# Kernel optimization log

Measured on AMD Instinct MI355X. Metric: run time of the kernel, lower is better.

## Reference

```python
import jax, jax.numpy as jnp
import numpy as np

D_STATE = 64
D_CONV = 5
HEADDIM = 64
EXPAND = 2


def setup_inputs() -> dict:
    key = jax.random.key(0)
    ks = jax.random.split(key, 12)
    b, ch, h, w = 4, 128, 64, 64
    d_inner = EXPAND * ch
    nheads = d_inner // HEADDIM
    conv_ch = d_inner + 2 * D_STATE
    d_in_proj = 2 * d_inner + 2 * D_STATE + nheads
    s = lambda k, shape, scale: jax.random.normal(k, shape, jnp.float32) * scale
    return {
        "noisy": s(ks[0], (b, ch, h, w), 1.0),
        "aux": s(ks[1], (b, ch, h, w), 1.0),
        "ln_gamma": jnp.ones((ch,), jnp.float32),
        "ln_beta": jnp.zeros((ch,), jnp.float32),
        "in_proj_w": s(ks[2], (d_in_proj, ch), ch ** -0.5),
        "conv_w": s(ks[3], (conv_ch, D_CONV), D_CONV ** -0.5),
        "conv_b": s(ks[4], (conv_ch,), 0.02),
        "A_log": jnp.log(jnp.linspace(1.0, 16.0, nheads)).astype(jnp.float32),
        "dt_bias": s(ks[5], (nheads,), 0.1),
        "D": jnp.ones((nheads,), jnp.float32),
        "rms_w": jnp.ones((d_inner,), jnp.float32),
        "out_proj_w": s(ks[6], (ch, d_inner), d_inner ** -0.5),
        "ff_w1": s(ks[7], (ch, ch, 3, 3), (ch * 9) ** -0.5),
        "ff_b1": jnp.zeros((ch,), jnp.float32),
        "ff_w2": s(ks[8], (ch, ch, 3, 3), (ch * 9) ** -0.5),
        "ff_b2": jnp.zeros((ch,), jnp.float32),
    }


def _mamba2(u, in_proj_w, conv_w, conv_b, A_log, dt_bias, D_skip, rms_w, out_proj_w):
    # u: (b, L, d_model). Mamba2 with ngroups=1, headdim=64.
    b, L, d = u.shape
    d_inner = EXPAND * d
    nheads = d_inner // HEADDIM
    zxbcdt = u @ in_proj_w.T  # (b, L, 2*d_inner + 2*d_state + nheads)
    z = zxbcdt[..., :d_inner]
    xBC = zxbcdt[..., d_inner:2 * d_inner + 2 * D_STATE]
    dt = jax.nn.softplus(zxbcdt[..., -nheads:] + dt_bias)  # (b, L, h)
    # causal depthwise conv1d along L + SiLU
    xBC_c = jnp.transpose(xBC, (0, 2, 1))  # (b, C, L)
    xBC_c = jax.lax.conv_general_dilated(
        xBC_c, conv_w[:, None, :], (1,), [(D_CONV - 1, 0)],
        feature_group_count=xBC_c.shape[1])
    xBC = jax.nn.silu(jnp.transpose(xBC_c + conv_b[None, :, None], (0, 2, 1)))
    x = xBC[..., :d_inner]
    B = xBC[..., d_inner:d_inner + D_STATE]  # (b, L, n)
    C = xBC[..., d_inner + D_STATE:]         # (b, L, n)
    A = -jnp.exp(A_log)                      # (h,)
    xh = x.reshape(b, L, nheads, HEADDIM)    # (b, L, h, p)
    dA = jnp.exp(dt * A)                     # (b, L, h)

    def step(hstate, inputs):
        dA_t, dt_t, x_t, B_t, C_t = inputs
        hstate = hstate * dA_t[:, :, None, None] + jnp.einsum('bh,bhp,bn->bhpn', dt_t, x_t, B_t)
        y_t = jnp.einsum('bhpn,bn->bhp', hstate, C_t)
        return hstate, y_t

    init = jnp.zeros((b, nheads, HEADDIM, D_STATE), u.dtype)
    xs = (jnp.moveaxis(dA, 1, 0), jnp.moveaxis(dt, 1, 0), jnp.moveaxis(xh, 1, 0),
          jnp.moveaxis(B, 1, 0), jnp.moveaxis(C, 1, 0))
    _, ys = jax.lax.scan(step, init, xs)
    y = jnp.moveaxis(ys, 0, 1) + xh * D_skip[None, None, :, None]  # (b, L, h, p)
    y = y.reshape(b, L, d_inner)
    # gated RMSNorm: rmsnorm(y * silu(z)) * weight
    y = y * jax.nn.silu(z)
    y = y * jax.lax.rsqrt(jnp.mean(y * y, axis=-1, keepdims=True) + 1e-5) * rms_w
    return y @ out_proj_w.T


def _conv3x3_reflect(x, w, b):
    x = jnp.pad(x, ((0, 0), (0, 0), (1, 1), (1, 1)), mode='reflect')
    return jax.lax.conv_general_dilated(x, w, (1, 1), 'VALID') + b[None, :, None, None]


def reference(noisy, aux, ln_gamma, ln_beta, in_proj_w, conv_w, conv_b, A_log,
              dt_bias, D, rms_w, out_proj_w, ff_w1, ff_b1, ff_w2, ff_b2):
    b, c, h, w = noisy.shape
    flat = jnp.transpose(noisy, (0, 2, 3, 1)).reshape(b, h * w, c)
    mu = jnp.mean(flat, axis=-1, keepdims=True)
    var = jnp.var(flat, axis=-1, keepdims=True)
    normed = (flat - mu) * jax.lax.rsqrt(var + 1e-5) * ln_gamma + ln_beta
    m = _mamba2(normed, in_proj_w, conv_w, conv_b, A_log, dt_bias, D, rms_w, out_proj_w)
    m = jnp.transpose(m.reshape(b, h, w, c), (0, 3, 1, 2))
    y = noisy + m
    ff = jax.nn.relu(_conv3x3_reflect(y, ff_w1, ff_b1))
    ff = jax.nn.relu(_conv3x3_reflect(ff, ff_w2, ff_b2))
    y = y + ff
    return (y, aux)
```

## Files before the change

### kernel.cpp

```cpp
#include <hip/hip_runtime.h>
#include <cstddef>

#define B_      4
#define C_      128
#define L_      4096
#define DIN     256
#define NH      4
#define HD      64
#define DS      64
#define CONVCH  384
#define DPROJ   644
#define CHUNK   64
#define NCHUNK  64

typedef short bf16x8 __attribute__((ext_vector_type(8)));
typedef float floatx16 __attribute__((ext_vector_type(16)));

__device__ __forceinline__ float siluf(float v) { return v / (1.f + __expf(-v)); }

__device__ __forceinline__ ushort f2bf(float v) {
  unsigned u = __float_as_uint(v);
  unsigned r = (u + 0x7fff + ((u >> 16) & 1)) >> 16;
  return (ushort)r;
}
__device__ __forceinline__ float bf2f(ushort h) {
  return __uint_as_float((unsigned)h << 16);
}

__device__ __forceinline__ void split8(float4 v0, float4 v1, bf16x8& hi, bf16x8& lo) {
  float f[8] = {v0.x, v0.y, v0.z, v0.w, v1.x, v1.y, v1.z, v1.w};
#pragma unroll
  for (int j = 0; j < 8; ++j) {
    ushort h = f2bf(f[j]);
    hi[j] = (short)h;
    lo[j] = (short)f2bf(f[j] - bf2f(h));
  }
}

__global__ __launch_bounds__(256) void wprep_all(
    const float* __restrict__ ipw, ushort* __restrict__ Bh, ushort* __restrict__ Bl,
    const float* __restrict__ opw, ushort* __restrict__ Oh, ushort* __restrict__ Ol,
    const float* __restrict__ fw1, ushort* __restrict__ Wt1,
    const float* __restrict__ fw2, ushort* __restrict__ Wt2) {
  int bi = blockIdx.x;
  int t = threadIdx.x;
  if (bi < 176) {
    int e = bi * 256 + t;
    int d = e >> 6;
    int c0 = (e & 63) * 2;
    int kk = c0 >> 4;
    int l = (d & 31) + 32 * ((c0 & 15) >> 3);
    int j = c0 & 7;
    size_t off = (((size_t)(d >> 5)) * 8 + kk) * 512 + l * 8 + j;
    float v0 = d < 644 ? ipw[(size_t)d * 128 + c0] : 0.f;
    float v1 = d < 644 ? ipw[(size_t)d * 128 + c0 + 1] : 0.f;
    ushort h0 = f2bf(v0), h1 = f2bf(v1);
    *(unsigned*)(Bh + off) = (unsigned)h0 | ((unsigned)h1 << 16);
    *(unsigned*)(Bl + off) = (unsigned)f2bf(v0 - bf2f(h0)) |
                             ((unsigned)f2bf(v1 - bf2f(h1)) << 16);
  } else if (bi < 304) {
    int e = (bi - 176) * 256 + t;
    int d = e >> 8;
    int c = e & 255;
    size_t f = ((size_t)(d >> 5) * 16 + (c >> 4)) * 512 +
               ((d & 31) + 32 * ((c & 15) >> 3)) * 8 + (c & 7);
    float v = opw[(size_t)d * 256 + c];
    ushort h = f2bf(v);
    Oh[f] = h;
    Ol[f] = f2bf(v - bf2f(h));
  } else {
    const float* fw = bi < 432 ? fw1 : fw2;
    ushort* Wt = bi < 432 ? Wt1 : Wt2;
    int co = (bi - 304) & 127;
    int cb = co >> 5;
    for (int e = t; e < 1152; e += 256) {
      int tap = e >> 7;
      int ci = e & 127;
      int kk = ci >> 4, k16 = ci & 15;
      int l = (co & 31) + 32 * (k16 >> 3);
      int off = ((tap * 8 + kk) * 4 + cb) * 512 + l * 8 + (k16 & 7);
      Wt[off] = f2bf(fw[(size_t)co * 1152 + ci * 9 + tap]);
    }
  }
}

__global__ __launch_bounds__(1024) void ln_gemm1(
    const float* __restrict__ noisy, const float* __restrict__ gamma,
    const float* __restrict__ beta,
    const ushort* __restrict__ Bh, const ushort* __restrict__ Bl,
    float* __restrict__ ZX) {
  int row = blockIdx.x, b = blockIdx.y;
  int t = threadIdx.x;
  __shared__ float tile[64 * 129];
  __shared__ float ps[16][64], pq[16][64];
  __shared__ float smu[64], srs[64];
  __shared__ __align__(16) ushort AhL[8192];
  __shared__ __align__(16) ushort AlL[8192];
  int px = t & 63, cg = t >> 6;
  float s = 0.f, s2 = 0.f;
  const float* src = noisy + ((size_t)b * C_) * L_ + row * 64;
  for (int i = 0; i < 8; ++i) {
    int c = cg * 8 + i;
    float v = src[(size_t)c * L_ + px];
    tile[px * 129 + c] = v;
    s += v; s2 += v * v;
  }
  ps[cg][px] = s; pq[cg][px] = s2;
  __syncthreads();
  if (t < 64) {
    float a = 0.f, qq = 0.f;
#pragma unroll
    for (int g = 0; g < 16; ++g) { a += ps[g][t]; qq += pq[g][t]; }
    float mu = a * (1.f / 128.f);
    float var = qq * (1.f / 128.f) - mu * mu;
    smu[t] = mu;
    srs[t] = rsqrtf(var + 1e-5f);
  }
  __syncthreads();
  for (int idx = t; idx < 4096; idx += 1024) {
    int p2 = idx >> 6;
    int c0 = (idx & 63) * 2;
    float v0 = (tile[p2 * 129 + c0] - smu[p2]) * srs[p2] * gamma[c0] + beta[c0];
    float v1 = (tile[p2 * 129 + c0 + 1] - smu[p2]) * srs[p2] * gamma[c0 + 1] + beta[c0 + 1];
    int kk = c0 >> 4;
    int l = (p2 & 31) + 32 * ((c0 & 15) >> 3);
    int j = c0 & 7;
    int off = ((p2 >> 5) * 8 + kk) * 512 + l * 8 + j;
    ushort h0 = f2bf(v0), h1 = f2bf(v1);
    *(unsigned*)(AhL + off) = (unsigned)h0 | ((unsigned)h1 << 16);
    *(unsigned*)(AlL + off) = (unsigned)f2bf(v0 - bf2f(h0)) |
                              ((unsigned)f2bf(v1 - bf2f(h1)) << 16);
  }
  __syncthreads();
  int wv = t >> 6, lane = t & 63;
  int db = wv & 1, pb = (wv >> 1) & 1, bq = wv >> 2;
  int rowadd = 4 * (lane >> 5);
  for (int bn = bq; bn < 11; bn += 4) {
    floatx16 acc;
#pragma unroll
    for (int i = 0; i < 16; ++i) acc[i] = 0.f;
    size_t bbase = ((size_t)(bn * 2 + db) * 8) * 64 + lane;
    const bf16x8* pBh = (const bf16x8*)Bh + bbase;
    const bf16x8* pBl = (const bf16x8*)Bl + bbase;
#pragma unroll
    for (int kk = 0; kk < 8; ++kk) {
      bf16x8 ah = *(const bf16x8*)(AhL + (pb * 8 + kk) * 512 + lane * 8);
      bf16x8 al = *(const bf16x8*)(AlL + (pb * 8 + kk) * 512 + lane * 8);
      bf16x8 bh = pBh[kk * 64];
      bf16x8 bl = pBl[kk * 64];
      acc = __builtin_amdgcn_mfma_f32_32x32x16_bf16(ah, bh, acc, 0, 0, 0);
      acc = __builtin_amdgcn_mfma_f32_32x32x16_bf16(al, bh, acc, 0, 0, 0);
      acc = __builtin_amdgcn_mfma_f32_32x32x16_bf16(ah, bl, acc, 0, 0, 0);
    }
    int d = bn * 64 + db * 32 + (lane & 31);
    if (d < 644) {
#pragma unroll
      for (int r = 0; r < 16; ++r) {
        int rowm = (r & 3) + 8 * (r >> 2) + rowadd;
        int pix = row * 64 + pb * 32 + rowm;
        ZX[((size_t)(b * L_ + pix)) * DPROJ + d] = acc[r];
      }
    }
  }
}

__global__ __launch_bounds__(384) void conv1d_silu(
    const float* __restrict__ ZX, const float* __restrict__ cw,
    const float* __restrict__ cb, float* __restrict__ XBC) {
  int ch = threadIdx.x;
  int l0 = blockIdx.x * 16, b = blockIdx.y;
  const float* base = ZX + ((size_t)b * L_) * DPROJ + DIN + ch;
  float w0 = cw[ch * 5], w1 = cw[ch * 5 + 1], w2 = cw[ch * 5 + 2],
        w3 = cw[ch * 5 + 3], w4 = cw[ch * 5 + 4];
  float bias = cb[ch];
  float win[20];
#pragma unroll
  for (int i = 0; i < 20; ++i) {
    int ll = l0 - 4 + i;
    win[i] = ll >= 0 ? base[(size_t)ll * DPROJ] : 0.f;
  }
  float* dst = XBC + ((size_t)(b * L_ + l0)) * CONVCH + ch;
#pragma unroll
  for (int j = 0; j < 16; ++j) {
    float acc = bias + w0 * win[j] + w1 * win[j + 1] + w2 * win[j + 2] +
                w3 * win[j + 3] + w4 * win[j + 4];
    dst[(size_t)j * CONVCH] = siluf(acc);
  }
}

#define UPDA(k, B4, C4) \
  st[4*k+0] = st[4*k+0]*da + cf*B4.x; y0 += st[4*k+0]*C4.x; \
  st[4*k+1] = st[4*k+1]*da + cf*B4.y; y1 += st[4*k+1]*C4.y; \
  st[4*k+2] = st[4*k+2]*da + cf*B4.z; y2 += st[4*k+2]*C4.z; \
  st[4*k+3] = st[4*k+3]*da + cf*B4.w; y3 += st[4*k+3]*C4.w;

__global__ __launch_bounds__(256, 4) void scan_passA(
    const float* __restrict__ XBC, const float* __restrict__ ZX,
    const float* __restrict__ dt_bias, const float* __restrict__ A_log,
    float* __restrict__ YL, float* __restrict__ SC, float* __restrict__ PC,
    float* __restrict__ CUM) {
  int chunk = blockIdx.x, h = blockIdx.y, b = blockIdx.z;
  int t = threadIdx.x;
  int p = t >> 2, q = t & 3;
  int bh = b * NH + h;
  __shared__ float sdt[CHUNK], sda[CHUNK];
  __shared__ float sB[32][64];
  __shared__ float sCc[32][64];
  __shared__ float sx[32][64];
  if (t < CHUNK) {
    int l = chunk * CHUNK + t;
    float v = ZX[((size_t)(b * L_ + l)) * DPROJ + 640 + h] + dt_bias[h];
    float dt = v > 20.f ? v : log1pf(expf(v));
    sdt[t] = dt;
    sda[t] = expf(dt * -expf(A_log[h]));
  }
  size_t rowbase = ((size_t)b * L_ + (size_t)chunk * CHUNK) * CONVCH;
  float* __restrict__ yl = YL + ((size_t)b * L_ + (size_t)chunk * CHUNK) * DIN + h * HD + p;
  float* __restrict__ cumout = CUM + (size_t)bh * L_ + chunk * CHUNK;
  float st[16];
#pragma unroll
  for (int j = 0; j < 16; ++j) st[j] = 0.f;
  float cum = 1.f;
  for (int half = 0; half < 2; ++half) {
    __syncthreads();
#pragma unroll
    for (int i = 0; i < 2; ++i) {
      int e = t + i * 256;
      int row = e >> 4, c4 = (e & 15) * 4;
      const float* gsrc = XBC + rowbase + (size_t)(half * 32 + row) * CONVCH;
      *(float4*)&sB[row][c4]  = *(const float4*)(gsrc + DIN + c4);
      *(float4*)&sCc[row][c4] = *(const float4*)(gsrc + DIN + DS + c4);
      *(float4*)&sx[row][c4]  = *(const float4*)(gsrc + h * HD + c4);
    }
    __syncthreads();
#pragma unroll 4
    for (int tl = 0; tl < 32; ++tl) {
      int tg = half * 32 + tl;
      float da = sda[tg], dtv = sdt[tg];
      float x = sx[tl][p];
      float cf = dtv * x;
      const float4* br = (const float4*)&sB[tl][q * 16];
      const float4* cr = (const float4*)&sCc[tl][q * 16];
      float4 B0 = br[0], B1 = br[1], B2 = br[2], B3 = br[3];
      float4 C0 = cr[0], C1 = cr[1], C2 = cr[2], C3 = cr[3];
      float y0 = 0.f, y1 = 0.f, y2 = 0.f, y3 = 0.f;
      UPDA(0, B0, C0) UPDA(1, B1, C1) UPDA(2, B2, C2) UPDA(3, B3, C3)
      float y = (y0 + y1) + (y2 + y3);
      y += __shfl_xor(y, 1);
      y += __shfl_xor(y, 2);
      cum *= da;
      if (q == 0) yl[(size_t)tg * DIN] = y;
      if (t == 0) cumout[tg] = cum;
    }
  }
  float* scp = SC + ((size_t)bh * NCHUNK + chunk) * 4096 + p * 64 + q * 16;
  *(float4*)(scp + 0)  = make_float4(st[0], st[1], st[2], st[3]);
  *(float4*)(scp + 4)  = make_float4(st[4], st[5], st[6], st[7]);
  *(float4*)(scp + 8)  = make_float4(st[8], st[9], st[10], st[11]);
  *(float4*)(scp + 12) = make_float4(st[12], st[13], st[14], st[15]);
  if (t == 0) PC[bh * NCHUNK + chunk] = cum;
}

__global__ __launch_bounds__(256) void scan_passB(
    float* __restrict__ SC, const float* __restrict__ PC) {
  int bh = blockIdx.x >> 4;
  int eg = blockIdx.x & 15;
  int e = eg * 256 + threadIdx.x;
  float h = 0.f;
#pragma unroll 8
  for (int c = 0; c < NCHUNK; ++c) {
    size_t idx = ((size_t)bh * NCHUNK + c) * 4096 + e;
    float s = SC[idx];
    float pcv = PC[bh * NCHUNK + c];
    SC[idx] = h;
    h = h * pcv + s;
  }
}

__global__ __launch_bounds__(1024) void passC_gate(
    const float* __restrict__ XBC, const float* __restrict__ SC,
    const float* __restrict__ CUM, const float* __restrict__ Dp,
    const float* __restrict__ YL, const float* __restrict__ ZX,
    const float* __restrict__ rmsw,
    const ushort* __restrict__ Oh, const ushort* __restrict__ Ol,
    const float* __restrict__ noisy, float* __restrict__ YRES) {
  __shared__ float yt[16384];
  __shared__ __align__(16) ushort fr[32768];
  int chunk = blockIdx.x, b = blockIdx.y;
  int t = threadIdx.x;
  int wv = t >> 6, lane = t & 63;
  size_t pix0g = (size_t)b * L_ + (size_t)chunk * CHUNK;
  float* sCcf  = (float*)fr;
  float* scumf = sCcf + 4096;

  float4 zr[4];
  {
    int lp = t & 31, slot2 = t >> 5;
#pragma unroll
    for (int it = 0; it < 2; ++it) {
      const float* z = ZX + (pix0g + it * 32 + slot2) * DPROJ;
      zr[it * 2]     = *(const float4*)(z + lp * 4);
      zr[it * 2 + 1] = *(const float4*)(z + 128 + lp * 4);
    }
  }
  for (int i = t; i < 4096; i += 1024) {
    *(float4*)&yt[i * 4] = *(const float4*)&YL[pix0g * DIN + (size_t)i * 4];
  }
  {
    int px = t >> 4, slot = t & 15;
    float4 cv = *(const float4*)(XBC + (pix0g + px) * CONVCH + DIN + DS + slot * 4);
    ((float4*)sCcf)[px * 16 + (slot ^ (px & 7))] = cv;
    if (t < 256) {
      int hh = t >> 6, px2 = t & 63;
      scumf[t] = CUM[((size_t)(b * NH + hh)) * L_ + chunk * CHUNK + px2];
    }
  }
  __syncthreads();

  {
    int px = t >> 4, c4 = (t & 15) * 4;
    const float* xs = XBC + (pix0g + px) * CONVCH;
#pragma unroll
    for (int hh = 0; hh < 4; ++hh) {
      float4 xv = *(const float4*)(xs + hh * HD + c4);
      float dv = Dp[hh];
      float* dst = &yt[px * 256 + hh * 64 + c4];
      dst[0] += xv.x * dv; dst[1] += xv.y * dv;
      dst[2] += xv.z * dv; dst[3] += xv.w * dv;
    }
  }
  __syncthreads();

  {
    int h1 = wv >> 2, ptile = (wv >> 1) & 1, pxtile = wv & 1;
    int arow = pxtile * 32 + (lane & 31);
    const float* Sb = SC + (((size_t)(b * NH + h1)) * NCHUNK + chunk) * 4096 +
                      (size_t)(ptile * 32 + (lane & 31)) * 64 + (lane >> 5) * 8;
    const float4* av = (const float4*)sCcf + arow * 16;
    int s0 = (lane >> 5) * 2;
    floatx16 acc;
#pragma unroll
    for (int i = 0; i < 16; ++i) acc[i] = 0.f;
#pragma unroll
    for (int kk = 0; kk < 4; ++kk) {
      float4 b0 = *(const float4*)(Sb + kk * 16);
      float4 b1 = *(const float4*)(Sb + kk * 16 + 4);
      int sa = kk * 4 + s0;
      float4 a0 = av[sa ^ (arow & 7)];
      float4 a1 = av[(sa + 1) ^ (arow & 7)];
      bf16x8 ah, al, bh, bl;
      split8(a0, a1, ah, al);
      split8(b0, b1, bh, bl);
      acc = __builtin_amdgcn_mfma_f32_32x32x16_bf16(ah, bh, acc, 0, 0, 0);
      acc = __builtin_amdgcn_mfma_f32_32x32x16_bf16(al, bh, acc, 0, 0, 0);
      acc = __builtin_amdgcn_mfma_f32_32x32x16_bf16(ah, bl, acc, 0, 0, 0);
    }
    int col = h1 * 64 + ptile * 32 + (lane & 31);
    int radd = 4 * (lane >> 5);
#pragma unroll
    for (int r = 0; r < 16; ++r) {
      int pxl = (r & 3) + 8 * (r >> 2) + radd;
      int px = pxtile * 32 + pxl;
      yt[px * 256 + col] += acc[r] * scumf[h1 * 64 + px];
    }
  }
  __syncthreads();

  ushort* AhL = fr;
  ushort* AlL = fr + 16384;
  {
    int lp = t & 31;
    int slot = t >> 5;
    float4 w0 = *(const float4*)(rmsw + lp * 4);
    float4 w1 = *(const float4*)(rmsw + 128 + lp * 4);
#pragma unroll
    for (int it = 0; it < 2; ++it) {
      int pl = it * 32 + slot;
      const float* y = &yt[pl * 256];
      float4 y0 = *(const float4*)(y + lp * 4);
      float4 y1 = *(const float4*)(y + 128 + lp * 4);
      float4 z0 = zr[it * 2];
      float4 z1 = zr[it * 2 + 1];
      float g[8];
      g[0] = y0.x * siluf(z0.x); g[1] = y0.y * siluf(z0.y);
      g[2] = y0.z * siluf(z0.z); g[3] = y0.w * siluf(z0.w);
      g[4] = y1.x * siluf(z1.x); g[5] = y1.y * siluf(z1.y);
      g[6] = y1.z * siluf(z1.z); g[7] = y1.w * siluf(z1.w);
      float ss = 0.f;
#pragma unroll
      for (int j = 0; j < 8; ++j) ss += g[j] * g[j];
      ss += __shfl_xor(ss, 16);
      ss += __shfl_xor(ss, 8);
      ss += __shfl_xor(ss, 4);
      ss += __shfl_xor(ss, 2);
      ss += __shfl_xor(ss, 1);
      float rs = rsqrtf(ss * (1.f / 256.f) + 1e-5f);
      float o[8];
      o[0] = g[0] * rs * w0.x; o[1] = g[1] * rs * w0.y;
      o[2] = g[2] * rs * w0.z; o[3] = g[3] * rs * w0.w;
      o[4] = g[4] * rs * w1.x; o[5] = g[5] * rs * w1.y;
      o[6] = g[6] * rs * w1.z; o[7] = g[7] * rs * w1.w;
#pragma unroll
      for (int grp = 0; grp < 2; ++grp) {
        int d = grp * 128 + lp * 4;
        int off = ((pl >> 5) * 16 + (d >> 4)) * 512 +
                  ((pl & 31) + 32 * ((d & 15) >> 3)) * 8 + (d & 7);
        ushort h0 = f2bf(o[grp*4+0]), h1 = f2bf(o[grp*4+1]);
        ushort h2 = f2bf(o[grp*4+2]), h3 = f2bf(o[grp*4+3]);
        uint2 hv, lv;
        hv.x = (unsigned)h0 | ((unsigned)h1 << 16);
        hv.y = (unsigned)h2 | ((unsigned)h3 << 16);
        lv.x = (unsigned)f2bf(o[grp*4+0] - bf2f(h0)) | ((unsigned)f2bf(o[grp*4+1] - bf2f(h1)) << 16);
        lv.y = (unsigned)f2bf(o[grp*4+2] - bf2f(h2)) | ((unsigned)f2bf(o[grp*4+3] - bf2f(h3)) << 16);
        *(uint2*)(AhL + off) = hv;
        *(uint2*)(AlL + off) = lv;
      }
    }
  }
  __syncthreads();

  floatx16 acc;
#pragma unroll
  for (int i = 0; i < 16; ++i) acc[i] = 0.f;
  int pb = wv >> 2, bn = (wv >> 1) & 1, db = wv & 1;
  int rowadd = 4 * (lane >> 5);
  if (wv < 8) {
    const bf16x8* pBh = (const bf16x8*)Oh;
    const bf16x8* pBl = (const bf16x8*)Ol;
    size_t bbase = ((size_t)(bn * 2 + db) * 16) * 64 + lane;
#pragma unroll
    for (int kk = 0; kk < 16; ++kk) {
      bf16x8 ah = *(const bf16x8*)(AhL + (pb * 16 + kk) * 512 + lane * 8);
      bf16x8 al = *(const bf16x8*)(AlL + (pb * 16 + kk) * 512 + lane * 8);
      bf16x8 bh = pBh[bbase + (size_t)kk * 64];
      bf16x8 bl = pBl[bbase + (size_t)kk * 64];
      acc = __builtin_amdgcn_mfma_f32_32x32x16_bf16(ah, bh, acc, 0, 0, 0);
      acc = __builtin_amdgcn_mfma_f32_32x32x16_bf16(al, bh, acc, 0, 0, 0);
      acc = __builtin_amdgcn_mfma_f32_32x32x16_bf16(ah, bl, acc, 0, 0, 0);
    }
  } else {
    int t2 = t - 512;
#pragma unroll
    for (int k = 0; k < 16; ++k) {
      int idx = t2 + k * 512;
      int c = idx >> 6, px = idx & 63;
      yt[idx] = noisy[((size_t)(b * C_ + c)) * L_ + chunk * CHUNK + px];
    }
  }
  __syncthreads();

  float* tile = (float*)fr;
  if (wv < 8) {
#pragma unroll
    for (int r = 0; r < 16; ++r) {
      int rowm = (r & 3) + 8 * (r >> 2) + rowadd;
      int rowp = pb * 32 + rowm;
      int col = bn * 64 + db * 32 + (lane & 31);
      tile[rowp * 129 + col] = acc[r];
    }
  }
  __syncthreads();
  for (int idx = t; idx < 8192; idx += 1024) {
    int c = idx >> 6, px = idx & 63;
    size_t o = ((size_t)(b * C_ + c)) * L_ + chunk * CHUNK + px;
    YRES[o] = yt[idx] + tile[px * 129 + c];
  }
}

template <int MODE>
__global__ __launch_bounds__(512) void conv3x3_direct(
    const void* __restrict__ inv, const ushort* __restrict__ Wt,
    const float* __restrict__ bias, const float* __restrict__ res,
    void* __restrict__ outv) {
  __shared__ __align__(16) ushort lds[3 * 64 * 128];
  int y = blockIdx.x, b = blockIdx.y;
  int t = threadIdx.x;
  int lane = t & 63;
  int wv = t >> 6;
  int ry[3];
  ry[0] = y == 0 ? 1 : y - 1;
  ry[1] = y;
  ry[2] = y == 63 ? 62 : y + 1;
  {
    int x = lane;
    for (int u = wv; u < 48; u += 8) {
      int r = u / 16;
      int cib = u % 16;
      int ci0 = cib * 8;
      ushort vals[8];
#pragma unroll
      for (int j = 0; j < 8; ++j) {
        size_t src = ((size_t)(b * C_ + ci0 + j)) * L_ + ry[r] * 64 + x;
        if (MODE == 0) vals[j] = f2bf(((const float*)inv)[src]);
        else           vals[j] = ((const ushort*)inv)[src];
      }
      int idx = (r * 64 + x) * 128 + (cib ^ (x & 15)) * 8;
      *(int4*)&lds[idx] = *(int4*)vals;
    }
  }
  __syncthreads();
  int cb = wv >> 1, nb = wv & 1;
  int n = lane & 31, hi = lane >> 5;
  floatx16 acc0, acc1;
#pragma unroll
  for (int i = 0; i < 16; ++i) { acc0[i] = 0.f; acc1[i] = 0.f; }
  const bf16x8* pW = (const bf16x8*)Wt;
  for (int tap = 0; tap < 9; ++tap) {
    int ky = tap / 3, kx = tap % 3;
    int xg = nb * 32 + n + kx - 1;
    int xx = xg < 0 ? 1 : (xg > 63 ? 62 : xg);
    int base = (ky * 64 + xx) * 128;
    int xs = xx & 15;
#pragma unroll
    for (int kk = 0; kk < 8; ++kk) {
      bf16x8 av = pW[(size_t)((tap * 8 + kk) * 4 + cb) * 64 + lane];
      bf16x8 bv = *(const bf16x8*)&lds[base + ((kk * 2 + hi) ^ xs) * 8];
      if (kk & 1) acc1 = __builtin_amdgcn_mfma_f32_32x32x16_bf16(av, bv, acc1, 0, 0, 0);
      else        acc0 = __builtin_amdgcn_mfma_f32_32x32x16_bf16(av, bv, acc0, 0, 0, 0);
    }
  }
  int x0 = nb * 32 + (lane & 31);
  int rowadd = 4 * (lane >> 5);
#pragma unroll
  for (int r = 0; r < 16; ++r) {
    int rowm = (r & 3) + 8 * (r >> 2) + rowadd;
    int co = cb * 32 + rowm;
    size_t o = ((size_t)(b * C_ + co)) * L_ + y * 64 + x0;
    float v = fmaxf(acc0[r] + acc1[r] + bias[co], 0.f);
    if (MODE == 0) {
      ((ushort*)outv)[o] = f2bf(v);
    } else {
      ((float*)outv)[o] = v + res[o];
    }
  }
}

extern "C" void kernel_launch(void* const* d_in, const int* in_sizes, int n_in,
                              void* d_out, int out_size, void* d_ws, size_t ws_size,
                              hipStream_t stream) {
  const float* noisy   = (const float*)d_in[0];
  const float* aux     = (const float*)d_in[1];
  const float* ln_g    = (const float*)d_in[2];
  const float* ln_b    = (const float*)d_in[3];
  const float* ipw     = (const float*)d_in[4];
  const float* cw      = (const float*)d_in[5];
  const float* cbv     = (const float*)d_in[6];
  const float* A_log   = (const float*)d_in[7];
  const float* dt_bias = (const float*)d_in[8];
  const float* Dp      = (const float*)d_in[9];
  const float* rmsw    = (const float*)d_in[10];
  const float* opw     = (const float*)d_in[11];
  const float* fw1     = (const float*)d_in[12];
  const float* fb1     = (const float*)d_in[13];
  const float* fw2     = (const float*)d_in[14];
  const float* fb2     = (const float*)d_in[15];
  float* out = (float*)d_out;
  float* ws  = (float*)d_ws;

  const size_t OFF_ZX   = 0;
  const size_t OFF_XBC  = OFF_ZX + 16384UL * 644;
  const size_t OFF_SCN  = OFF_XBC + 16384UL * 384;
  const size_t OFF_WT   = OFF_SCN + 4194304UL;
  const size_t OFF_WO   = OFF_WT + 73728UL;
  const size_t OFF_CUM  = OFF_WT + 131072UL;
  const size_t OFF_YL   = OFF_CUM + 65536UL;
  const size_t OFF_PC   = OFF_YL + 16384UL * 256;
  const size_t OFF_WT2  = OFF_PC + 1024UL;
  const size_t OFF_YRES = OFF_WT2 + 73728UL;

  float* ZX   = ws + OFF_ZX;
  float* XBC  = ws + OFF_XBC;
  float* SC   = ws + OFF_SCN;
  float* CUM  = ws + OFF_CUM;
  float* YL   = ws + OFF_YL;
  float* PC   = ws + OFF_PC;
  ushort* Bnh  = (ushort*)(ws + OFF_YL);
  ushort* Bnl  = Bnh + 45056UL * 2;
  ushort* Wt1 = (ushort*)(ws + OFF_WT);
  ushort* Woh  = (ushort*)(ws + OFF_WO);
  ushort* Wol  = Woh + 32768UL;
  ushort* Wt2 = (ushort*)(ws + OFF_WT2);
  ushort* FF1 = (ushort*)(ws + OFF_SCN);
  float* YRES = ws + OFF_YRES;

  wprep_all<<<560, 256, 0, stream>>>(ipw, Bnh, Bnl, opw, Woh, Wol, fw1, Wt1, fw2, Wt2);
  ln_gemm1<<<dim3(64, 4), 1024, 0, stream>>>(noisy, ln_g, ln_b, Bnh, Bnl, ZX);
  conv1d_silu<<<dim3(L_ / 16, B_), 384, 0, stream>>>(ZX, cw, cbv, XBC);
  scan_passA<<<dim3(NCHUNK, NH, B_), 256, 0, stream>>>(XBC, ZX, dt_bias, A_log, YL, SC, PC, CUM);
  scan_passB<<<256, 256, 0, stream>>>(SC, PC);
  passC_gate<<<dim3(NCHUNK, B_), 1024, 0, stream>>>(XBC, SC, CUM, Dp, YL, ZX,
                                                    rmsw, Woh, Wol, noisy, YRES);
  conv3x3_direct<0><<<dim3(64, 4), 512, 0, stream>>>(YRES, Wt1, fb1, nullptr, FF1);
  conv3x3_direct<1><<<dim3(64, 4), 512, 0, stream>>>(FF1, Wt2, fb2, YRES, out);
  hipMemcpyAsync(out + 2097152, aux, 2097152UL * sizeof(float),
                 hipMemcpyDeviceToDevice, stream);
}
```

Before: 244.3 us.

## Fuse causal conv1d into scan pass A and fold aux copy into conv3x3

The depthwise causal conv1d+SiLU is merged into the chunk scan kernel. Each 1024-thread block stages a 68-row window of ZX in LDS, computes the conv output for all 384 channels, and runs the four heads' scans from LDS, so XBC no longer makes a global round trip before the scan. Only the x and C columns are still written to XBC for the later pass. The aux passthrough memcpy becomes a second z-slice of the final conv3x3 launch, removing a separate copy. The trade-off is about 150KB of LDS per block, fewer and larger blocks (256 in total), and redundant conv work on the 4-row halo.

Measured after the change: 281.7 us. 1.15x slower.

```diff
diff --git a/kernel.cpp b/kernel.cpp
--- a/kernel.cpp
+++ b/kernel.cpp
@@ -12,6 +12,7 @@
 #define DPROJ   644
 #define CHUNK   64
 #define NCHUNK  64
+#define ZSTRIDE 388
 
 typedef short bf16x8 __attribute__((ext_vector_type(8)));
 typedef float floatx16 __attribute__((ext_vector_type(16)));
@@ -164,83 +165,86 @@
   }
 }
 
-__global__ __launch_bounds__(384) void conv1d_silu(
-    const float* __restrict__ ZX, const float* __restrict__ cw,
-    const float* __restrict__ cb, float* __restrict__ XBC) {
-  int ch = threadIdx.x;
-  int l0 = blockIdx.x * 16, b = blockIdx.y;
-  const float* base = ZX + ((size_t)b * L_) * DPROJ + DIN + ch;
-  float w0 = cw[ch * 5], w1 = cw[ch * 5 + 1], w2 = cw[ch * 5 + 2],
-        w3 = cw[ch * 5 + 3], w4 = cw[ch * 5 + 4];
-  float bias = cb[ch];
-  float win[20];
-#pragma unroll
-  for (int i = 0; i < 20; ++i) {
-    int ll = l0 - 4 + i;
-    win[i] = ll >= 0 ? base[(size_t)ll * DPROJ] : 0.f;
-  }
-  float* dst = XBC + ((size_t)(b * L_ + l0)) * CONVCH + ch;
-#pragma unroll
-  for (int j = 0; j < 16; ++j) {
-    float acc = bias + w0 * win[j] + w1 * win[j + 1] + w2 * win[j + 2] +
-                w3 * win[j + 3] + w4 * win[j + 4];
-    dst[(size_t)j * CONVCH] = siluf(acc);
-  }
-}
-
 #define UPDA(k, B4, C4) \
   st[4*k+0] = st[4*k+0]*da + cf*B4.x; y0 += st[4*k+0]*C4.x; \
   st[4*k+1] = st[4*k+1]*da + cf*B4.y; y1 += st[4*k+1]*C4.y; \
   st[4*k+2] = st[4*k+2]*da + cf*B4.z; y2 += st[4*k+2]*C4.z; \
   st[4*k+3] = st[4*k+3]*da + cf*B4.w; y3 += st[4*k+3]*C4.w;
 
-__global__ __launch_bounds__(256, 4) void scan_passA(
-    const float* __restrict__ XBC, const float* __restrict__ ZX,
-    const float* __restrict__ dt_bias, const float* __restrict__ A_log,
-    float* __restrict__ YL, float* __restrict__ SC, float* __restrict__ PC,
-    float* __restrict__ CUM) {
-  int chunk = blockIdx.x, h = blockIdx.y, b = blockIdx.z;
+__global__ __launch_bounds__(1024) void conv_scanA(
+    const float* __restrict__ ZX, const float* __restrict__ cw,
+    const float* __restrict__ cb, const float* __restrict__ dt_bias,
+    const float* __restrict__ A_log,
+    float* __restrict__ XBC, float* __restrict__ YL, float* __restrict__ SC,
+    float* __restrict__ PC, float* __restrict__ CUM) {
+  __shared__ float zst[68 * ZSTRIDE];
+  __shared__ float sxbc[32 * ZSTRIDE];
+  __shared__ float sda[4][64], sdt[4][64];
+  int chunk = blockIdx.x, b = blockIdx.y;
   int t = threadIdx.x;
-  int p = t >> 2, q = t & 3;
+  int h = t >> 8, t1 = t & 255;
+  int p = t1 >> 2, q = t1 & 3;
   int bh = b * NH + h;
-  __shared__ float sdt[CHUNK], sda[CHUNK];
-  __shared__ float sB[32][64];
-  __shared__ float sCc[32][64];
-  __shared__ float sx[32][64];
-  if (t < CHUNK) {
-    int l = chunk * CHUNK + t;
-    float v = ZX[((size_t)(b * L_ + l)) * DPROJ + 640 + h] + dt_bias[h];
-    float dt = v > 20.f ? v : log1pf(expf(v));
-    sdt[t] = dt;
-    sda[t] = expf(dt * -expf(A_log[h]));
-  }
-  size_t rowbase = ((size_t)b * L_ + (size_t)chunk * CHUNK) * CONVCH;
-  float* __restrict__ yl = YL + ((size_t)b * L_ + (size_t)chunk * CHUNK) * DIN + h * HD + p;
-  float* __restrict__ cumout = CUM + (size_t)bh * L_ + chunk * CHUNK;
+  int l0 = chunk * CHUNK;
+  size_t pix0g = (size_t)b * L_ + l0;
+  float* __restrict__ yl = YL + pix0g * DIN + h * HD + p;
+  float* __restrict__ cumout = CUM + (size_t)bh * L_ + l0;
+
+  {
+    for (int i = 0; i < 7; ++i) {
+      int idx = t + i * 1024;
+      if (idx < 6596) {
+        int r = idx / 97, c4 = idx - r * 97;
+        int g = l0 - 4 + r;
+        float4 v = make_float4(0.f, 0.f, 0.f, 0.f);
+        if (g >= 0)
+          v = *(const float4*)(ZX + ((size_t)b * L_ + g) * DPROJ + 256 + c4 * 4);
+        *(float4*)&zst[r * ZSTRIDE + c4 * 4] = v;
+      }
+    }
+  }
+  __syncthreads();
+  if (t < 256) {
+    int hh = t >> 6, tl = t & 63;
+    float vraw = zst[(tl + 4) * ZSTRIDE + 384 + hh] + dt_bias[hh];
+    float dt = vraw > 20.f ? vraw : log1pf(expf(vraw));
+    sdt[hh][tl] = dt;
+    sda[hh][tl] = expf(dt * -expf(A_log[hh]));
+  }
+
   float st[16];
 #pragma unroll
   for (int j = 0; j < 16; ++j) st[j] = 0.f;
   float cum = 1.f;
+
   for (int half = 0; half < 2; ++half) {
-    __syncthreads();
-#pragma unroll
-    for (int i = 0; i < 2; ++i) {
-      int e = t + i * 256;
-      int row = e >> 4, c4 = (e & 15) * 4;
-      const float* gsrc = XBC + rowbase + (size_t)(half * 32 + row) * CONVCH;
-      *(float4*)&sB[row][c4]  = *(const float4*)(gsrc + DIN + c4);
-      *(float4*)&sCc[row][c4] = *(const float4*)(gsrc + DIN + DS + c4);
-      *(float4*)&sx[row][c4]  = *(const float4*)(gsrc + h * HD + c4);
+    if (half) __syncthreads();
+#pragma unroll
+    for (int i = 0; i < 12; ++i) {
+      int e = t + i * 1024;
+      int px = e / 384, ch = e - px * 384;
+      int r0 = half * 32 + px;
+      const float* wp = cw + ch * 5;
+      float acc = cb[ch];
+      acc += wp[0] * zst[(r0 + 0) * ZSTRIDE + ch];
+      acc += wp[1] * zst[(r0 + 1) * ZSTRIDE + ch];
+      acc += wp[2] * zst[(r0 + 2) * ZSTRIDE + ch];
+      acc += wp[3] * zst[(r0 + 3) * ZSTRIDE + ch];
+      acc += wp[4] * zst[(r0 + 4) * ZSTRIDE + ch];
+      float v = siluf(acc);
+      sxbc[px * ZSTRIDE + ch] = v;
+      if (ch < 256 || ch >= 320)
+        XBC[(pix0g + half * 32 + px) * CONVCH + ch] = v;
     }
     __syncthreads();
 #pragma unroll 4
     for (int tl = 0; tl < 32; ++tl) {
       int tg = half * 32 + tl;
-      float da = sda[tg], dtv = sdt[tg];
-      float x = sx[tl][p];
+      float da = sda[h][tg], dtv = sdt[h][tg];
+      float x = sxbc[tl * ZSTRIDE + h * HD + p];
       float cf = dtv * x;
-      const float4* br = (const float4*)&sB[tl][q * 16];
-      const float4* cr = (const float4*)&sCc[tl][q * 16];
+      const float4* br = (const float4*)&sxbc[tl * ZSTRIDE + 256 + q * 16];
+      const float4* cr = (const float4*)&sxbc[tl * ZSTRIDE + 320 + q * 16];
       float4 B0 = br[0], B1 = br[1], B2 = br[2], B3 = br[3];
       float4 C0 = cr[0], C1 = cr[1], C2 = cr[2], C3 = cr[3];
       float y0 = 0.f, y1 = 0.f, y2 = 0.f, y3 = 0.f;
@@ -250,7 +254,7 @@
       y += __shfl_xor(y, 2);
       cum *= da;
       if (q == 0) yl[(size_t)tg * DIN] = y;
-      if (t == 0) cumout[tg] = cum;
+      if (t1 == 0) cumout[tg] = cum;
     }
   }
   float* scp = SC + ((size_t)bh * NCHUNK + chunk) * 4096 + p * 64 + q * 16;
@@ -258,7 +262,7 @@
   *(float4*)(scp + 4)  = make_float4(st[4], st[5], st[6], st[7]);
   *(float4*)(scp + 8)  = make_float4(st[8], st[9], st[10], st[11]);
   *(float4*)(scp + 12) = make_float4(st[12], st[13], st[14], st[15]);
-  if (t == 0) PC[bh * NCHUNK + chunk] = cum;
+  if (t1 == 0) PC[bh * NCHUNK + chunk] = cum;
 }
 
 __global__ __launch_bounds__(256) void scan_passB(
@@ -471,10 +475,18 @@
 __global__ __launch_bounds__(512) void conv3x3_direct(
     const void* __restrict__ inv, const ushort* __restrict__ Wt,
     const float* __restrict__ bias, const float* __restrict__ res,
-    void* __restrict__ outv) {
-  __shared__ __align__(16) ushort lds[3 * 64 * 128];
+    void* __restrict__ outv, const float* __restrict__ aux) {
   int y = blockIdx.x, b = blockIdx.y;
   int t = threadIdx.x;
+  if (MODE == 1 && blockIdx.z == 1) {
+    const float4* s = (const float4*)aux;
+    float4* d = (float4*)((float*)outv + 2097152);
+    int base = (b * 64 + y) * 512 + t;
+#pragma unroll
+    for (int k = 0; k < 4; ++k) d[base + k * 131072] = s[base + k * 131072];
+    return;
+  }
+  __shared__ __align__(16) ushort lds[3 * 64 * 128];
   int lane = t & 63;
   int wv = t >> 6;
   int ry[3];
@@ -585,13 +597,11 @@
 
   wprep_all<<<560, 256, 0, stream>>>(ipw, Bnh, Bnl, opw, Woh, Wol, fw1, Wt1, fw2, Wt2);
   ln_gemm1<<<dim3(64, 4), 1024, 0, stream>>>(noisy, ln_g, ln_b, Bnh, Bnl, ZX);
-  conv1d_silu<<<dim3(L_ / 16, B_), 384, 0, stream>>>(ZX, cw, cbv, XBC);
-  scan_passA<<<dim3(NCHUNK, NH, B_), 256, 0, stream>>>(XBC, ZX, dt_bias, A_log, YL, SC, PC, CUM);
+  conv_scanA<<<dim3(NCHUNK, B_), 1024, 0, stream>>>(ZX, cw, cbv, dt_bias, A_log,
+                                                    XBC, YL, SC, PC, CUM);
   scan_passB<<<256, 256, 0, stream>>>(SC, PC);
   passC_gate<<<dim3(NCHUNK, B_), 1024, 0, stream>>>(XBC, SC, CUM, Dp, YL, ZX,
                                                     rmsw, Woh, Wol, noisy, YRES);
-  conv3x3_direct<0><<<dim3(64, 4), 512, 0, stream>>>(YRES, Wt1, fb1, nullptr, FF1);
-  conv3x3_direct<1><<<dim3(64, 4), 512, 0, stream>>>(FF1, Wt2, fb2, YRES, out);
-  hipMemcpyAsync(out + 2097152, aux, 2097152UL * sizeof(float),
-                 hipMemcpyDeviceToDevice, stream);
-}
+  conv3x3_direct<0><<<dim3(64, 4), 512, 0, stream>>>(YRES, Wt1, fb1, nullptr, FF1, nullptr);
+  conv3x3_direct<1><<<dim3(64, 4, 2), 512, 0, stream>>>(FF1, Wt2, fb2, YRES, out, aux);
+}
```
